# Performance work log

Hardware: AMD Instinct MI355X
Metric: run time of the kernel (lower is better)

The kernel has to match this reference:

```python
import jax, jax.numpy as jnp
import numpy as np

N_NODES = 50000
N_EDGES = 1_600_000
IN_C, HID_C, OUT_C = 512, 256, 50
ALPHA = 0.1
NUM_LAYERS = 10


def setup_inputs() -> dict:
    key = jax.random.key(0)
    ks = jax.random.split(key, 8)
    x = jax.random.normal(ks[0], (N_NODES, IN_C), dtype=jnp.float32)
    edge_row = jax.random.randint(ks[1], (N_EDGES,), 0, N_NODES, dtype=jnp.int32)
    edge_col = jax.random.randint(ks[2], (N_EDGES,), 0, N_NODES, dtype=jnp.int32)
    edge_weight = jax.random.uniform(ks[3], (N_EDGES,), dtype=jnp.float32)
    s1 = 1.0 / np.sqrt(IN_C)
    s2 = 1.0 / np.sqrt(HID_C)
    W1 = jax.random.uniform(ks[4], (IN_C, HID_C), minval=-s1, maxval=s1, dtype=jnp.float32)
    b1 = jax.random.uniform(ks[5], (HID_C,), minval=-s1, maxval=s1, dtype=jnp.float32)
    W2 = jax.random.uniform(ks[6], (HID_C, OUT_C), minval=-s2, maxval=s2, dtype=jnp.float32)
    b2 = jax.random.uniform(ks[7], (OUT_C,), minval=-s2, maxval=s2, dtype=jnp.float32)
    return {"x": x, "edge_row": edge_row, "edge_col": edge_col,
            "edge_weight": edge_weight, "W1": W1, "b1": b1, "W2": W2, "b2": b2}


def reference(x, edge_row, edge_col, edge_weight, W1, b1, W2, b2):
    # MLP: Linear -> ReLU -> Linear (dropout inactive in eval, no batch norm)
    h = jax.nn.relu(x @ W1 + b1)          # [N, HID_C]
    h = h @ W2 + b2                        # [N, OUT_C]
    x0 = h

    def spmm(v):
        # out[i] = sum_{e: row[e]==i} w[e] * v[col[e]]
        msgs = v[edge_col] * edge_weight[:, None]   # [E, OUT_C]
        return jax.ops.segment_sum(msgs, edge_row, num_segments=N_NODES)

    def step(h, _):
        h = spmm(h) * (1.0 - ALPHA) + ALPHA * x0
        return h, None

    h, _ = jax.lax.scan(step, h, None, length=NUM_LAYERS)
    return jax.nn.log_softmax(h, axis=1)
```

## Files before the change

kernel.cpp:

```cpp
#include <hip/hip_runtime.h>
#include <cstddef>
#include <cstdint>
#include <math.h>

#define N_NODES 50000
#define N_EDGES 1600000
#define IN_C 512
#define HID_C 256
#define OUT_C 50
#define PAD_C 64
#define NUM_LAYERS 10
#define NBUCK 98
#define BSHIFT 9
#define BCAP 20480
#define PHB_CHUNK 8192
#define PHB_BLOCKS 196

typedef __attribute__((ext_vector_type(8))) short short8;
typedef __attribute__((ext_vector_type(4))) float floatx4;

__device__ inline unsigned short f2bf(float f) {
    unsigned int u = __float_as_uint(f);
    u += 0x7fffu + ((u >> 16) & 1u);
    return (unsigned short)(u >> 16);
}

__device__ inline unsigned cvtpk(float lo, float hi) {
    unsigned r;
    asm("v_cvt_pk_bf16_f32 %0, %1, %2" : "=v"(r) : "v"(lo), "v"(hi));
    return r;
}

__device__ inline short8 pack_bf16x8(float4 lo, float4 hi) {
    union { unsigned u[4]; short8 s; } r;
    r.u[0] = cvtpk(lo.x, lo.y);
    r.u[1] = cvtpk(lo.z, lo.w);
    r.u[2] = cvtpk(hi.x, hi.y);
    r.u[3] = cvtpk(hi.z, hi.w);
    return r.s;
}

#define ASYNC16(g, l)                                                     \
    __builtin_amdgcn_global_load_lds(                                     \
        (const __attribute__((address_space(1))) void*)(g),               \
        (__attribute__((address_space(3))) void*)(l), 16, 0, 0)

#define WAITCNT6() asm volatile("s_waitcnt vmcnt(6)" ::: "memory")
#define WAITCNT0() asm volatile("s_waitcnt vmcnt(0)" ::: "memory")
#define SBAR()     __builtin_amdgcn_s_barrier()

__global__ __launch_bounds__(256) void transpose_w1(const float* __restrict__ W1,
                                                    unsigned short* __restrict__ Wt) {
    __shared__ float tile[32][33];
    int bx = blockIdx.x;
    int by = blockIdx.y;
    int tx = threadIdx.x & 31, ty = threadIdx.x >> 5;
#pragma unroll
    for (int i = 0; i < 32; i += 8)
        tile[ty + i][tx] = W1[(bx * 32 + ty + i) * HID_C + by * 32 + tx];
    __syncthreads();
#pragma unroll
    for (int i = 0; i < 32; i += 8)
        Wt[(size_t)(by * 32 + ty + i) * IN_C + bx * 32 + tx] = f2bf(tile[tx][ty + i]);
}

__global__ void pad_w2(const float* __restrict__ W2, const float* __restrict__ b2,
                       unsigned short* __restrict__ Wpt, float* __restrict__ bp) {
    int idx = blockIdx.x * blockDim.x + threadIdx.x;
    if (idx < PAD_C * HID_C) {
        int n = idx >> 8, k = idx & 255;
        float v = (n < OUT_C) ? W2[k * OUT_C + n] : 0.f;
        Wpt[idx] = f2bf(v);
    }
    if (idx < PAD_C) bp[idx] = (idx < OUT_C) ? b2[idx] : 0.f;
}

__global__ __launch_bounds__(256) void gemm1_fused(const float* __restrict__ A,
                                                   const unsigned short* __restrict__ Wt,
                                                   const float* __restrict__ b1,
                                                   const unsigned short* __restrict__ Wpt,
                                                   const float* __restrict__ bp,
                                                   float* __restrict__ h0f,
                                                   unsigned short* __restrict__ h0b) {
    __shared__ __align__(16) char smem[73728];
    float*          Ab[3] = {(float*)smem,
                             (float*)(smem + 24576),
                             (float*)(smem + 49152)};
    unsigned short* Bb[3] = {(unsigned short*)(smem + 8192),
                             (unsigned short*)(smem + 32768),
                             (unsigned short*)(smem + 57344)};
    unsigned short* Hs = (unsigned short*)smem;
    const int HS_LD = 264;

    const int tid  = threadIdx.x;
    const int wave = tid >> 6, lane = tid & 63;
    const int quad = lane >> 4, l16 = lane & 15;
    const int m0 = blockIdx.x * 64;
    const int wm = (wave >> 1) * 32;
    const int wn = (wave & 1) * 128;

    floatx4 acc[2][8];
#pragma unroll
    for (int i = 0; i < 2; ++i)
#pragma unroll
        for (int j = 0; j < 8; ++j) acc[i][j] = (floatx4){0.f, 0.f, 0.f, 0.f};

    const int ar = (tid >> 3), ac = tid & 7;
    auto stage = [&](int bi, int ks) {
        const int k0 = ks << 5;
#pragma unroll
        for (int j = 0; j < 2; ++j) {
            int slot = tid + j * 256;
            int r = slot >> 3, c = slot & 7;
            int gr = m0 + r;
            if (gr >= N_NODES) gr = N_NODES - 1;
            const float* src = A + (size_t)gr * IN_C + k0 + ((c ^ (r & 7)) << 2);
            ASYNC16(src, Ab[bi] + (slot << 2));
        }
#pragma unroll
        for (int j = 0; j < 4; ++j) {
            const unsigned short* src = Wt + (size_t)tid * IN_C + k0 + (j << 3);
            ASYNC16(src, Bb[bi] + (j << 11) + (tid << 3));
        }
    };

    auto compute = [&](int bi) {
        const float* As_ = Ab[bi];
        const unsigned short* Bs_ = Bb[bi];
        short8 bfr[8], afr[2];
#pragma unroll
        for (int nt = 0; nt < 8; ++nt)
            bfr[nt] = *(const short8*)&Bs_[(quad << 11) + ((wn + nt * 16 + l16) << 3)];
#pragma unroll
        for (int mt = 0; mt < 2; ++mt) {
            int r  = wm + mt * 16 + l16;
            int rx = r & 7;
            float4 lo = *(const float4*)&As_[(r << 5) + (((2 * quad)     ^ rx) << 2)];
            float4 hi = *(const float4*)&As_[(r << 5) + (((2 * quad + 1) ^ rx) << 2)];
            afr[mt] = pack_bf16x8(lo, hi);
        }
#pragma unroll
        for (int mt = 0; mt < 2; ++mt)
#pragma unroll
            for (int nt = 0; nt < 8; ++nt)
                acc[mt][nt] = __builtin_amdgcn_mfma_f32_16x16x32_bf16(afr[mt], bfr[nt],
                                                                      acc[mt][nt], 0, 0, 0);
    };

    stage(0, 0);
    stage(1, 1);
#pragma unroll
    for (int ks = 0; ks < 14; ++ks) {
        WAITCNT6();
        SBAR();
        stage((ks + 2) % 3, ks + 2);
        compute(ks % 3);
    }
    WAITCNT6(); SBAR(); compute(2);
    WAITCNT0(); SBAR(); compute(0);
    __syncthreads();

#pragma unroll
    for (int nt = 0; nt < 8; ++nt) {
        int n = wn + nt * 16 + l16;
        float bn = b1[n];
#pragma unroll
        for (int mt = 0; mt < 2; ++mt)
#pragma unroll
            for (int r = 0; r < 4; ++r) {
                float v = acc[mt][nt][r] + bn;
                v = v > 0.f ? v : 0.f;
                Hs[(wm + mt * 16 + quad * 4 + r) * HS_LD + n] = f2bf(v);
            }
    }
    __syncthreads();

    floatx4 acc2[4];
#pragma unroll
    for (int nt = 0; nt < 4; ++nt) acc2[nt] = (floatx4){0.f, 0.f, 0.f, 0.f};
    const int hrow = (wave << 4) + l16;
#pragma unroll
    for (int k2 = 0; k2 < 8; ++k2) {
        short8 haf = *(const short8*)&Hs[hrow * HS_LD + (k2 << 5) + (quad << 3)];
#pragma unroll
        for (int nt = 0; nt < 4; ++nt) {
            short8 bf = *(const short8*)&Wpt[(size_t)((nt << 4) + l16) * HID_C + (k2 << 5) + (quad << 3)];
            acc2[nt] = __builtin_amdgcn_mfma_f32_16x16x32_bf16(haf, bf, acc2[nt], 0, 0, 0);
        }
    }
#pragma unroll
    for (int nt = 0; nt < 4; ++nt) {
        int c = (nt << 4) + l16;
        float bn = bp[c];
#pragma unroll
        for (int r = 0; r < 4; ++r) {
            int row = m0 + (wave << 4) + (quad << 2) + r;
            if (row < N_NODES) {
                float v = acc2[nt][r] + bn;
                h0f[(size_t)row * PAD_C + c] = v;
                h0b[(size_t)row * PAD_C + c] = f2bf(v);
            }
        }
    }
}

__global__ __launch_bounds__(256) void bucket_scatter(const int* __restrict__ erow,
                                                      const int* __restrict__ ecol,
                                                      const float* __restrict__ ew,
                                                      int* __restrict__ bfill,
                                                      uint2* __restrict__ buckets) {
    __shared__ int lcnt[NBUCK];
    __shared__ int lbase[NBUCK];
    const int t = threadIdx.x;
    for (int b = t; b < NBUCK; b += 256) lcnt[b] = 0;
    __syncthreads();
    const int e0 = blockIdx.x * PHB_CHUNK;
    const int e1 = min(e0 + PHB_CHUNK, N_EDGES);
    for (int e = e0 + t; e < e1; e += 256)
        atomicAdd(&lcnt[erow[e] >> BSHIFT], 1);
    __syncthreads();
    for (int b = t; b < NBUCK; b += 256) {
        lbase[b] = atomicAdd(&bfill[b], lcnt[b]);
        lcnt[b] = 0;
    }
    __syncthreads();
    for (int e = e0 + t; e < e1; e += 256) {
        int r = erow[e];
        int b = r >> BSHIFT;
        int o = atomicAdd(&lcnt[b], 1);
        int idx = lbase[b] + o;
        if (idx < BCAP) {
            unsigned packed = ((unsigned)(r - (b << BSHIFT)) << 17) | (unsigned)ecol[e];
            buckets[(size_t)b * BCAP + idx] = make_uint2(packed, __float_as_uint(ew[e]));
        }
    }
}

__global__ __launch_bounds__(128) void bucket_scan(const int* __restrict__ bfill,
                                                   int* __restrict__ bbase,
                                                   int* __restrict__ rowptr) {
    __shared__ int sd[128];
    int t = threadIdx.x;
    int v = (t < NBUCK) ? min(bfill[t], BCAP) : 0;
    sd[t] = v;
    __syncthreads();
    for (int off = 1; off < 128; off <<= 1) {
        int x = (t >= off) ? sd[t - off] : 0;
        __syncthreads();
        sd[t] += x;
        __syncthreads();
    }
    if (t < NBUCK) bbase[t] = sd[t] - v;
    if (t == NBUCK - 1) {
        bbase[NBUCK] = sd[t];
        rowptr[N_NODES] = sd[t];
    }
}

__global__ __launch_bounds__(256) void bucket_csr(const uint2* __restrict__ buckets,
                                                  const int* __restrict__ bfill,
                                                  const int* __restrict__ bbase,
                                                  int* __restrict__ rowptr,
                                                  uint2* __restrict__ edges) {
    __shared__ int hist[512];
    __shared__ int excl[512];
    __shared__ int psum[256];
    const int b = blockIdx.x;
    const int t = threadIdx.x;
    const int n = min(bfill[b], BCAP);
    const uint2* bk = buckets + (size_t)b * BCAP;

    hist[t] = 0; hist[t + 256] = 0;
    __syncthreads();
    for (int i = t; i < n; i += 256)
        atomicAdd(&hist[bk[i].x >> 17], 1);
    __syncthreads();
    int a0 = hist[2 * t], a1 = hist[2 * t + 1];
    psum[t] = a0 + a1;
    __syncthreads();
    for (int off = 1; off < 256; off <<= 1) {
        int x = (t >= off) ? psum[t - off] : 0;
        __syncthreads();
        psum[t] += x;
        __syncthreads();
    }
    int pe = psum[t] - (a0 + a1);
    excl[2 * t] = pe;
    excl[2 * t + 1] = pe + a0;
    __syncthreads();
    const int base = bbase[b];
#pragma unroll
    for (int k = 0; k < 2; ++k) {
        int lr = t + k * 256;
        int r = (b << BSHIFT) + lr;
        if (r < N_NODES) rowptr[r] = base + excl[lr];
    }
    hist[t] = 0; hist[t + 256] = 0;
    __syncthreads();
    for (int i = t; i < n; i += 256) {
        uint2 ed = bk[i];
        int lr = ed.x >> 17;
        int pos = base + excl[lr] + atomicAdd(&hist[lr], 1);
        edges[pos] = make_uint2(ed.x & 0x1FFFFu, ed.y);
    }
}

__device__ inline void edge_fma(float* acc, float wgt, uint4 hv) {
    acc[0] = fmaf(wgt, __uint_as_float(hv.x << 16),         acc[0]);
    acc[1] = fmaf(wgt, __uint_as_float(hv.x & 0xffff0000u), acc[1]);
    acc[2] = fmaf(wgt, __uint_as_float(hv.y << 16),         acc[2]);
    acc[3] = fmaf(wgt, __uint_as_float(hv.y & 0xffff0000u), acc[3]);
    acc[4] = fmaf(wgt, __uint_as_float(hv.z << 16),         acc[4]);
    acc[5] = fmaf(wgt, __uint_as_float(hv.z & 0xffff0000u), acc[5]);
    acc[6] = fmaf(wgt, __uint_as_float(hv.w << 16),         acc[6]);
    acc[7] = fmaf(wgt, __uint_as_float(hv.w & 0xffff0000u), acc[7]);
}

template <bool LAST>
__global__ __launch_bounds__(256) void prop8(const int* __restrict__ rowptr,
                                             const uint2* __restrict__ edges,
                                             const unsigned short* __restrict__ hin,
                                             const float* __restrict__ h0f,
                                             unsigned short* __restrict__ hout_b,
                                             float* __restrict__ out_f) {
    int wid = (blockIdx.x * blockDim.x + threadIdx.x) >> 6;
    if (wid >= N_NODES) return;
    int lane = threadIdx.x & 63;
    int slot = lane >> 3;
    int lc   = lane & 7;
    int s = rowptr[wid], e = rowptr[wid + 1];

    float acc0[8], acc1[8];
#pragma unroll
    for (int k = 0; k < 8; ++k) { acc0[k] = 0.f; acc1[k] = 0.f; }

    int i = s;
    for (; i + 32 <= e; i += 32) {
        uint2 cw0 = edges[i + slot];
        uint2 cw1 = edges[i + 8 + slot];
        uint2 cw2 = edges[i + 16 + slot];
        uint2 cw3 = edges[i + 24 + slot];
        uint4 hv0 = *(const uint4*)((const char*)hin + ((size_t)cw0.x << 7) + lc * 16);
        uint4 hv1 = *(const uint4*)((const char*)hin + ((size_t)cw1.x << 7) + lc * 16);
        uint4 hv2 = *(const uint4*)((const char*)hin + ((size_t)cw2.x << 7) + lc * 16);
        uint4 hv3 = *(const uint4*)((const char*)hin + ((size_t)cw3.x << 7) + lc * 16);
        edge_fma(acc0, __uint_as_float(cw0.y), hv0);
        edge_fma(acc1, __uint_as_float(cw1.y), hv1);
        edge_fma(acc0, __uint_as_float(cw2.y), hv2);
        edge_fma(acc1, __uint_as_float(cw3.y), hv3);
    }
    for (; i + 16 <= e; i += 16) {
        uint2 cw0 = edges[i + slot];
        uint2 cw1 = edges[i + 8 + slot];
        uint4 hv0 = *(const uint4*)((const char*)hin + ((size_t)cw0.x << 7) + lc * 16);
        uint4 hv1 = *(const uint4*)((const char*)hin + ((size_t)cw1.x << 7) + lc * 16);
        edge_fma(acc0, __uint_as_float(cw0.y), hv0);
        edge_fma(acc1, __uint_as_float(cw1.y), hv1);
    }
    for (; i < e; i += 8) {
        int idx = i + slot;
        uint2 cw = (idx < e) ? edges[idx] : make_uint2(0u, 0u);
        float wgt = (idx < e) ? __uint_as_float(cw.y) : 0.f;
        uint4 hv = *(const uint4*)((const char*)hin + ((size_t)cw.x << 7) + lc * 16);
        edge_fma(acc0, wgt, hv);
    }

    float r[8];
#pragma unroll
    for (int k = 0; k < 8; ++k) {
        float v = acc0[k] + acc1[k];
        v += __shfl_xor(v, 8, 64);
        v += __shfl_xor(v, 16, 64);
        v += __shfl_xor(v, 32, 64);
        r[k] = v;
    }

    size_t off = (size_t)wid * PAD_C + lc * 8;
    float4 h0a = *(const float4*)(h0f + off);
    float4 h0b4 = *(const float4*)(h0f + off + 4);
    r[0] = 0.9f * r[0] + 0.1f * h0a.x;  r[1] = 0.9f * r[1] + 0.1f * h0a.y;
    r[2] = 0.9f * r[2] + 0.1f * h0a.z;  r[3] = 0.9f * r[3] + 0.1f * h0a.w;
    r[4] = 0.9f * r[4] + 0.1f * h0b4.x; r[5] = 0.9f * r[5] + 0.1f * h0b4.y;
    r[6] = 0.9f * r[6] + 0.1f * h0b4.z; r[7] = 0.9f * r[7] + 0.1f * h0b4.w;

    if (!LAST) {
        if (slot == 0) {
            uint4 u;
            u.x = ((unsigned)f2bf(r[1]) << 16) | f2bf(r[0]);
            u.y = ((unsigned)f2bf(r[3]) << 16) | f2bf(r[2]);
            u.z = ((unsigned)f2bf(r[5]) << 16) | f2bf(r[4]);
            u.w = ((unsigned)f2bf(r[7]) << 16) | f2bf(r[6]);
            *(uint4*)((char*)hout_b + ((size_t)wid << 7) + lc * 16) = u;
        }
    } else {
        int ch0 = lc * 8;
        float m = -INFINITY;
#pragma unroll
        for (int k = 0; k < 8; ++k) if (ch0 + k < OUT_C) m = fmaxf(m, r[k]);
        m = fmaxf(m, __shfl_xor(m, 1, 64));
        m = fmaxf(m, __shfl_xor(m, 2, 64));
        m = fmaxf(m, __shfl_xor(m, 4, 64));
        float ss = 0.f;
#pragma unroll
        for (int k = 0; k < 8; ++k) if (ch0 + k < OUT_C) ss += __expf(r[k] - m);
        ss += __shfl_xor(ss, 1, 64);
        ss += __shfl_xor(ss, 2, 64);
        ss += __shfl_xor(ss, 4, 64);
        float lse = __logf(ss);
        if (slot == 0) {
#pragma unroll
            for (int k = 0; k < 8; ++k)
                if (ch0 + k < OUT_C)
                    out_f[(size_t)wid * OUT_C + ch0 + k] = (r[k] - m) - lse;
        }
    }
}

extern "C" void kernel_launch(void* const* d_in, const int* in_sizes, int n_in,
                              void* d_out, int out_size, void* d_ws, size_t ws_size,
                              hipStream_t stream) {
    const float* x    = (const float*)d_in[0];
    const int*   erow = (const int*)d_in[1];
    const int*   ecol = (const int*)d_in[2];
    const float* ew   = (const float*)d_in[3];
    const float* W1   = (const float*)d_in[4];
    const float* b1   = (const float*)d_in[5];
    const float* W2   = (const float*)d_in[6];
    const float* b2   = (const float*)d_in[7];
    float* out = (float*)d_out;

    char* p = (char*)d_ws;
    auto alloc = [&](size_t bytes) {
        char* r = p;
        p += (bytes + 255) & ~(size_t)255;
        return r;
    };
    char*  scratch = alloc((size_t)NBUCK * BCAP * 8);
    float* h0f    = (float*)alloc((size_t)N_NODES * PAD_C * 4);
    unsigned short* h0b = (unsigned short*)alloc((size_t)N_NODES * PAD_C * 2);
    uint2* edges  = (uint2*)alloc((size_t)N_EDGES * 8);
    int*   rowptr = (int*)alloc((size_t)(N_NODES + 1) * 4);
    int*   bfill  = (int*)alloc((size_t)NBUCK * 4);
    int*   bbase  = (int*)alloc((size_t)(NBUCK + 1) * 4);
    float* bp     = (float*)alloc((size_t)PAD_C * 4);
    unsigned short* Wt  = (unsigned short*)alloc((size_t)HID_C * IN_C * 2);
    unsigned short* Wpt = (unsigned short*)alloc((size_t)PAD_C * HID_C * 2);
    uint2* buckets = (uint2*)scratch;
    unsigned short* ha = (unsigned short*)scratch;
    unsigned short* hb = (unsigned short*)(scratch + (size_t)N_NODES * PAD_C * 2);

    hipMemsetAsync(bfill, 0, (size_t)NBUCK * 4, stream);

    bucket_scatter<<<PHB_BLOCKS, 256, 0, stream>>>(erow, ecol, ew, bfill, buckets);
    bucket_scan<<<1, 128, 0, stream>>>(bfill, bbase, rowptr);
    bucket_csr<<<NBUCK, 256, 0, stream>>>(buckets, bfill, bbase, rowptr, edges);

    transpose_w1<<<dim3(IN_C / 32, HID_C / 32), 256, 0, stream>>>(W1, Wt);
    pad_w2<<<(PAD_C * HID_C + 255) / 256, 256, 0, stream>>>(W2, b2, Wpt, bp);
    gemm1_fused<<<(N_NODES + 63) / 64, 256, 0, stream>>>(x, Wt, b1, Wpt, bp, h0f, h0b);

    const int prop_blocks = (N_NODES * 64 + 255) / 256;
    const unsigned short* cur = h0b;
    unsigned short* nxt = ha;
    for (int l = 0; l < NUM_LAYERS - 1; ++l) {
        prop8<false><<<prop_blocks, 256, 0, stream>>>(rowptr, edges, cur, h0f,
                                                      nxt, nullptr);
        const unsigned short* t = nxt;
        nxt = (nxt == ha) ? hb : ha;
        cur = t;
    }
    prop8<true><<<prop_blocks, 256, 0, stream>>>(rowptr, edges, cur, h0f,
                                                 nullptr, out);
}
```

Before: 624.6 us.

## Split propagation features into two 32-channel halves processed by separate passes

Stores the bf16 feature table as two 32-channel halves and runs each non-final propagation layer as two kernels, one per half. The aim is a 3.2 MB gather table per pass that fits better in cache, with 64-byte rows instead of 128-byte rows. In exchange every layer reads the edge list twice and launches twice as many kernels. The change also swizzles the W1 tile layout in shared memory to cut bank conflicts and switches edge reads to nontemporal loads.

New measurement: 850.3 us. 36.1% more time.

```diff
diff --git a/kernel.cpp b/kernel.cpp
--- a/kernel.cpp
+++ b/kernel.cpp
@@ -9,6 +9,7 @@
 #define HID_C 256
 #define OUT_C 50
 #define PAD_C 64
+#define HALF_C 32
 #define NUM_LAYERS 10
 #define NBUCK 98
 #define BSHIFT 9
@@ -81,7 +82,8 @@
                                                    const unsigned short* __restrict__ Wpt,
                                                    const float* __restrict__ bp,
                                                    float* __restrict__ h0f,
-                                                   unsigned short* __restrict__ h0b) {
+                                                   unsigned short* __restrict__ hA0,
+                                                   unsigned short* __restrict__ hB0) {
     __shared__ __align__(16) char smem[73728];
     float*          Ab[3] = {(float*)smem,
                              (float*)(smem + 24576),
@@ -105,7 +107,6 @@
 #pragma unroll
         for (int j = 0; j < 8; ++j) acc[i][j] = (floatx4){0.f, 0.f, 0.f, 0.f};
 
-    const int ar = (tid >> 3), ac = tid & 7;
     auto stage = [&](int bi, int ks) {
         const int k0 = ks << 5;
 #pragma unroll
@@ -119,8 +120,11 @@
         }
 #pragma unroll
         for (int j = 0; j < 4; ++j) {
-            const unsigned short* src = Wt + (size_t)tid * IN_C + k0 + (j << 3);
-            ASYNC16(src, Bb[bi] + (j << 11) + (tid << 3));
+            int slot = tid + j * 256;
+            int n = slot >> 2, c = slot & 3;
+            int cs = c ^ ((n >> 1) & 3);
+            const unsigned short* src = Wt + (size_t)n * IN_C + k0 + (cs << 3);
+            ASYNC16(src, Bb[bi] + (slot << 3));
         }
     };
 
@@ -129,8 +133,11 @@
         const unsigned short* Bs_ = Bb[bi];
         short8 bfr[8], afr[2];
 #pragma unroll
-        for (int nt = 0; nt < 8; ++nt)
-            bfr[nt] = *(const short8*)&Bs_[(quad << 11) + ((wn + nt * 16 + l16) << 3)];
+        for (int nt = 0; nt < 8; ++nt) {
+            int n  = wn + nt * 16 + l16;
+            int cq = quad ^ ((n >> 1) & 3);
+            bfr[nt] = *(const short8*)&Bs_[(n << 5) + (cq << 3)];
+        }
 #pragma unroll
         for (int mt = 0; mt < 2; ++mt) {
             int r  = wm + mt * 16 + l16;
@@ -198,7 +205,9 @@
             if (row < N_NODES) {
                 float v = acc2[nt][r] + bn;
                 h0f[(size_t)row * PAD_C + c] = v;
-                h0b[(size_t)row * PAD_C + c] = f2bf(v);
+                unsigned short vb = f2bf(v);
+                if (c < HALF_C) hA0[(size_t)row * HALF_C + c] = vb;
+                else            hB0[(size_t)row * HALF_C + (c - HALF_C)] = vb;
             }
         }
     }
@@ -316,52 +325,104 @@
     acc[7] = fmaf(wgt, __uint_as_float(hv.w & 0xffff0000u), acc[7]);
 }
 
-template <bool LAST>
-__global__ __launch_bounds__(256) void prop8(const int* __restrict__ rowptr,
-                                             const uint2* __restrict__ edges,
-                                             const unsigned short* __restrict__ hin,
-                                             const float* __restrict__ h0f,
-                                             unsigned short* __restrict__ hout_b,
-                                             float* __restrict__ out_f) {
+__global__ __launch_bounds__(256) void prop_half(const int* __restrict__ rowptr,
+                                                 const uint2* __restrict__ edges,
+                                                 const unsigned short* __restrict__ hin,
+                                                 const float* __restrict__ h0f,
+                                                 const int hoff,
+                                                 unsigned short* __restrict__ hout) {
+    int wid = (blockIdx.x * blockDim.x + threadIdx.x) >> 6;
+    if (wid >= N_NODES) return;
+    int lane = threadIdx.x & 63;
+    int slot = lane >> 2;
+    int lc2  = lane & 3;
+    int s = rowptr[wid], e = rowptr[wid + 1];
+    const unsigned long long* e8 = (const unsigned long long*)edges;
+
+    float acc0[8], acc1[8];
+#pragma unroll
+    for (int k = 0; k < 8; ++k) { acc0[k] = 0.f; acc1[k] = 0.f; }
+
+    int i = s;
+    for (; i + 32 <= e; i += 32) {
+        unsigned long long c0 = __builtin_nontemporal_load(e8 + i + slot);
+        unsigned long long c1 = __builtin_nontemporal_load(e8 + i + 16 + slot);
+        uint4 hv0 = *(const uint4*)((const char*)hin + (((size_t)(unsigned)c0) << 6) + lc2 * 16);
+        uint4 hv1 = *(const uint4*)((const char*)hin + (((size_t)(unsigned)c1) << 6) + lc2 * 16);
+        edge_fma(acc0, __uint_as_float((unsigned)(c0 >> 32)), hv0);
+        edge_fma(acc1, __uint_as_float((unsigned)(c1 >> 32)), hv1);
+    }
+    for (; i < e; i += 16) {
+        int idx = i + slot;
+        unsigned long long c0 = (idx < e) ? __builtin_nontemporal_load(e8 + idx) : 0ull;
+        float wgt = (idx < e) ? __uint_as_float((unsigned)(c0 >> 32)) : 0.f;
+        uint4 hv = *(const uint4*)((const char*)hin + (((size_t)(unsigned)c0) << 6) + lc2 * 16);
+        edge_fma(acc0, wgt, hv);
+    }
+
+    float r[8];
+#pragma unroll
+    for (int k = 0; k < 8; ++k) {
+        float v = acc0[k] + acc1[k];
+        v += __shfl_xor(v, 4, 64);
+        v += __shfl_xor(v, 8, 64);
+        v += __shfl_xor(v, 16, 64);
+        v += __shfl_xor(v, 32, 64);
+        r[k] = v;
+    }
+
+    size_t off = (size_t)wid * PAD_C + hoff + lc2 * 8;
+    float4 h0a  = *(const float4*)(h0f + off);
+    float4 h0b4 = *(const float4*)(h0f + off + 4);
+    r[0] = 0.9f * r[0] + 0.1f * h0a.x;  r[1] = 0.9f * r[1] + 0.1f * h0a.y;
+    r[2] = 0.9f * r[2] + 0.1f * h0a.z;  r[3] = 0.9f * r[3] + 0.1f * h0a.w;
+    r[4] = 0.9f * r[4] + 0.1f * h0b4.x; r[5] = 0.9f * r[5] + 0.1f * h0b4.y;
+    r[6] = 0.9f * r[6] + 0.1f * h0b4.z; r[7] = 0.9f * r[7] + 0.1f * h0b4.w;
+
+    if (slot == 0) {
+        uint4 u;
+        u.x = ((unsigned)f2bf(r[1]) << 16) | f2bf(r[0]);
+        u.y = ((unsigned)f2bf(r[3]) << 16) | f2bf(r[2]);
+        u.z = ((unsigned)f2bf(r[5]) << 16) | f2bf(r[4]);
+        u.w = ((unsigned)f2bf(r[7]) << 16) | f2bf(r[6]);
+        *(uint4*)((char*)hout + ((size_t)wid << 6) + lc2 * 16) = u;
+    }
+}
+
+__global__ __launch_bounds__(256) void prop_last(const int* __restrict__ rowptr,
+                                                 const uint2* __restrict__ edges,
+                                                 const unsigned short* __restrict__ hinA,
+                                                 const unsigned short* __restrict__ hinB,
+                                                 const float* __restrict__ h0f,
+                                                 float* __restrict__ out_f) {
     int wid = (blockIdx.x * blockDim.x + threadIdx.x) >> 6;
     if (wid >= N_NODES) return;
     int lane = threadIdx.x & 63;
     int slot = lane >> 3;
     int lc   = lane & 7;
+    const unsigned short* hbase = (lc < 4) ? hinA : hinB;
+    const int lco = lc & 3;
     int s = rowptr[wid], e = rowptr[wid + 1];
+    const unsigned long long* e8 = (const unsigned long long*)edges;
 
     float acc0[8], acc1[8];
 #pragma unroll
     for (int k = 0; k < 8; ++k) { acc0[k] = 0.f; acc1[k] = 0.f; }
 
     int i = s;
-    for (; i + 32 <= e; i += 32) {
-        uint2 cw0 = edges[i + slot];
-        uint2 cw1 = edges[i + 8 + slot];
-        uint2 cw2 = edges[i + 16 + slot];
-        uint2 cw3 = edges[i + 24 + slot];
-        uint4 hv0 = *(const uint4*)((const char*)hin + ((size_t)cw0.x << 7) + lc * 16);
-        uint4 hv1 = *(const uint4*)((const char*)hin + ((size_t)cw1.x << 7) + lc * 16);
-        uint4 hv2 = *(const uint4*)((const char*)hin + ((size_t)cw2.x << 7) + lc * 16);
-        uint4 hv3 = *(const uint4*)((const char*)hin + ((size_t)cw3.x << 7) + lc * 16);
-        edge_fma(acc0, __uint_as_float(cw0.y), hv0);
-        edge_fma(acc1, __uint_as_float(cw1.y), hv1);
-        edge_fma(acc0, __uint_as_float(cw2.y), hv2);
-        edge_fma(acc1, __uint_as_float(cw3.y), hv3);
-    }
     for (; i + 16 <= e; i += 16) {
-        uint2 cw0 = edges[i + slot];
-        uint2 cw1 = edges[i + 8 + slot];
-        uint4 hv0 = *(const uint4*)((const char*)hin + ((size_t)cw0.x << 7) + lc * 16);
-        uint4 hv1 = *(const uint4*)((const char*)hin + ((size_t)cw1.x << 7) + lc * 16);
-        edge_fma(acc0, __uint_as_float(cw0.y), hv0);
-        edge_fma(acc1, __uint_as_float(cw1.y), hv1);
+        unsigned long long c0 = __builtin_nontemporal_load(e8 + i + slot);
+        unsigned long long c1 = __builtin_nontemporal_load(e8 + i + 8 + slot);
+        uint4 hv0 = *(const uint4*)((const char*)hbase + (((size_t)(unsigned)c0) << 6) + lco * 16);
+        uint4 hv1 = *(const uint4*)((const char*)hbase + (((size_t)(unsigned)c1) << 6) + lco * 16);
+        edge_fma(acc0, __uint_as_float((unsigned)(c0 >> 32)), hv0);
+        edge_fma(acc1, __uint_as_float((unsigned)(c1 >> 32)), hv1);
     }
     for (; i < e; i += 8) {
         int idx = i + slot;
-        uint2 cw = (idx < e) ? edges[idx] : make_uint2(0u, 0u);
-        float wgt = (idx < e) ? __uint_as_float(cw.y) : 0.f;
-        uint4 hv = *(const uint4*)((const char*)hin + ((size_t)cw.x << 7) + lc * 16);
+        unsigned long long c0 = (idx < e) ? __builtin_nontemporal_load(e8 + idx) : 0ull;
+        float wgt = (idx < e) ? __uint_as_float((unsigned)(c0 >> 32)) : 0.f;
+        uint4 hv = *(const uint4*)((const char*)hbase + (((size_t)(unsigned)c0) << 6) + lco * 16);
         edge_fma(acc0, wgt, hv);
     }
 
@@ -376,43 +437,32 @@
     }
 
     size_t off = (size_t)wid * PAD_C + lc * 8;
-    float4 h0a = *(const float4*)(h0f + off);
+    float4 h0a  = *(const float4*)(h0f + off);
     float4 h0b4 = *(const float4*)(h0f + off + 4);
     r[0] = 0.9f * r[0] + 0.1f * h0a.x;  r[1] = 0.9f * r[1] + 0.1f * h0a.y;
     r[2] = 0.9f * r[2] + 0.1f * h0a.z;  r[3] = 0.9f * r[3] + 0.1f * h0a.w;
     r[4] = 0.9f * r[4] + 0.1f * h0b4.x; r[5] = 0.9f * r[5] + 0.1f * h0b4.y;
     r[6] = 0.9f * r[6] + 0.1f * h0b4.z; r[7] = 0.9f * r[7] + 0.1f * h0b4.w;
 
-    if (!LAST) {
-        if (slot == 0) {
-            uint4 u;
-            u.x = ((unsigned)f2bf(r[1]) << 16) | f2bf(r[0]);
-            u.y = ((unsigned)f2bf(r[3]) << 16) | f2bf(r[2]);
-            u.z = ((unsigned)f2bf(r[5]) << 16) | f2bf(r[4]);
-            u.w = ((unsigned)f2bf(r[7]) << 16) | f2bf(r[6]);
-            *(uint4*)((char*)hout_b + ((size_t)wid << 7) + lc * 16) = u;
-        }
-    } else {
-        int ch0 = lc * 8;
-        float m = -INFINITY;
-#pragma unroll
-        for (int k = 0; k < 8; ++k) if (ch0 + k < OUT_C) m = fmaxf(m, r[k]);
-        m = fmaxf(m, __shfl_xor(m, 1, 64));
-        m = fmaxf(m, __shfl_xor(m, 2, 64));
-        m = fmaxf(m, __shfl_xor(m, 4, 64));
-        float ss = 0.f;
-#pragma unroll
-        for (int k = 0; k < 8; ++k) if (ch0 + k < OUT_C) ss += __expf(r[k] - m);
-        ss += __shfl_xor(ss, 1, 64);
-        ss += __shfl_xor(ss, 2, 64);
-        ss += __shfl_xor(ss, 4, 64);
-        float lse = __logf(ss);
-        if (slot == 0) {
-#pragma unroll
-            for (int k = 0; k < 8; ++k)
-                if (ch0 + k < OUT_C)
-                    out_f[(size_t)wid * OUT_C + ch0 + k] = (r[k] - m) - lse;
-        }
+    int ch0 = lc * 8;
+    float m = -INFINITY;
+#pragma unroll
+    for (int k = 0; k < 8; ++k) if (ch0 + k < OUT_C) m = fmaxf(m, r[k]);
+    m = fmaxf(m, __shfl_xor(m, 1, 64));
+    m = fmaxf(m, __shfl_xor(m, 2, 64));
+    m = fmaxf(m, __shfl_xor(m, 4, 64));
+    float ss = 0.f;
+#pragma unroll
+    for (int k = 0; k < 8; ++k) if (ch0 + k < OUT_C) ss += __expf(r[k] - m);
+    ss += __shfl_xor(ss, 1, 64);
+    ss += __shfl_xor(ss, 2, 64);
+    ss += __shfl_xor(ss, 4, 64);
+    float lse = __logf(ss);
+    if (slot == 0) {
+#pragma unroll
+        for (int k = 0; k < 8; ++k)
+            if (ch0 + k < OUT_C)
+                out_f[(size_t)wid * OUT_C + ch0 + k] = (r[k] - m) - lse;
     }
 }
 
@@ -435,9 +485,9 @@
         p += (bytes + 255) & ~(size_t)255;
         return r;
     };
+    const size_t HTAB = (size_t)N_NODES * HALF_C * 2;
     char*  scratch = alloc((size_t)NBUCK * BCAP * 8);
     float* h0f    = (float*)alloc((size_t)N_NODES * PAD_C * 4);
-    unsigned short* h0b = (unsigned short*)alloc((size_t)N_NODES * PAD_C * 2);
     uint2* edges  = (uint2*)alloc((size_t)N_EDGES * 8);
     int*   rowptr = (int*)alloc((size_t)(N_NODES + 1) * 4);
     int*   bfill  = (int*)alloc((size_t)NBUCK * 4);
@@ -446,8 +496,10 @@
     unsigned short* Wt  = (unsigned short*)alloc((size_t)HID_C * IN_C * 2);
     unsigned short* Wpt = (unsigned short*)alloc((size_t)PAD_C * HID_C * 2);
     uint2* buckets = (uint2*)scratch;
-    unsigned short* ha = (unsigned short*)scratch;
-    unsigned short* hb = (unsigned short*)(scratch + (size_t)N_NODES * PAD_C * 2);
+    unsigned short* hAt[2] = {(unsigned short*)scratch,
+                              (unsigned short*)(scratch + HTAB)};
+    unsigned short* hBt[2] = {(unsigned short*)(scratch + 2 * HTAB),
+                              (unsigned short*)(scratch + 3 * HTAB)};
 
     hipMemsetAsync(bfill, 0, (size_t)NBUCK * 4, stream);
 
@@ -457,18 +509,19 @@
 
     transpose_w1<<<dim3(IN_C / 32, HID_C / 32), 256, 0, stream>>>(W1, Wt);
     pad_w2<<<(PAD_C * HID_C + 255) / 256, 256, 0, stream>>>(W2, b2, Wpt, bp);
-    gemm1_fused<<<(N_NODES + 63) / 64, 256, 0, stream>>>(x, Wt, b1, Wpt, bp, h0f, h0b);
+    gemm1_fused<<<(N_NODES + 63) / 64, 256, 0, stream>>>(x, Wt, b1, Wpt, bp,
+                                                         h0f, hAt[0], hBt[0]);
 
     const int prop_blocks = (N_NODES * 64 + 255) / 256;
-    const unsigned short* cur = h0b;
-    unsigned short* nxt = ha;
+    int cur = 0;
     for (int l = 0; l < NUM_LAYERS - 1; ++l) {
-        prop8<false><<<prop_blocks, 256, 0, stream>>>(rowptr, edges, cur, h0f,
-                                                      nxt, nullptr);
-        const unsigned short* t = nxt;
-        nxt = (nxt == ha) ? hb : ha;
-        cur = t;
-    }
-    prop8<true><<<prop_blocks, 256, 0, stream>>>(rowptr, edges, cur, h0f,
-                                                 nullptr, out);
-}
+        int nxt = cur ^ 1;
+        prop_half<<<prop_blocks, 256, 0, stream>>>(rowptr, edges, hAt[cur], h0f,
+                                                   0, hAt[nxt]);
+        prop_half<<<prop_blocks, 256, 0, stream>>>(rowptr, edges, hBt[cur], h0f,
+                                                   HALF_C, hBt[nxt]);
+        cur = nxt;
+    }
+    prop_last<<<prop_blocks, 256, 0, stream>>>(rowptr, edges, hAt[cur], hBt[cur],
+                                               h0f, out);
+}
```

## Fuse ten propagation layers into one persistent kernel with grid barriers

Applied to the files above, without the earlier changes.

Replaces the ten per-layer prop8 launches with a single persistent kernel of 1024 blocks that loops over the layers. Waves stride over nodes, and blocks synchronise between layers through an atomic-counter grid barrier. The teacher term now reads the bf16 h0 instead of the fp32 h0, and the W1 shared-memory tile layout gets an XOR swizzle. This removes launch overhead and per-layer tail gaps, but adds barrier spin cost and depends on all blocks being co-resident; using bf16 h0 also costs a little precision.

Measured after the change: 2.285 ms. 3.66x slower.

```diff
diff --git a/kernel.cpp b/kernel.cpp
--- a/kernel.cpp
+++ b/kernel.cpp
@@ -15,6 +15,8 @@
 #define BCAP 20480
 #define PHB_CHUNK 8192
 #define PHB_BLOCKS 196
+#define PROP_BLOCKS 1024
+#define PROP_WAVES (PROP_BLOCKS * 4)
 
 typedef __attribute__((ext_vector_type(8))) short short8;
 typedef __attribute__((ext_vector_type(4))) float floatx4;
@@ -105,7 +107,6 @@
 #pragma unroll
         for (int j = 0; j < 8; ++j) acc[i][j] = (floatx4){0.f, 0.f, 0.f, 0.f};
 
-    const int ar = (tid >> 3), ac = tid & 7;
     auto stage = [&](int bi, int ks) {
         const int k0 = ks << 5;
 #pragma unroll
@@ -119,8 +120,11 @@
         }
 #pragma unroll
         for (int j = 0; j < 4; ++j) {
-            const unsigned short* src = Wt + (size_t)tid * IN_C + k0 + (j << 3);
-            ASYNC16(src, Bb[bi] + (j << 11) + (tid << 3));
+            int slot = tid + j * 256;
+            int n = slot >> 2, c = slot & 3;
+            int cs = c ^ ((n >> 1) & 3);
+            const unsigned short* src = Wt + (size_t)n * IN_C + k0 + (cs << 3);
+            ASYNC16(src, Bb[bi] + (slot << 3));
         }
     };
 
@@ -129,8 +133,11 @@
         const unsigned short* Bs_ = Bb[bi];
         short8 bfr[8], afr[2];
 #pragma unroll
-        for (int nt = 0; nt < 8; ++nt)
-            bfr[nt] = *(const short8*)&Bs_[(quad << 11) + ((wn + nt * 16 + l16) << 3)];
+        for (int nt = 0; nt < 8; ++nt) {
+            int n  = wn + nt * 16 + l16;
+            int cq = quad ^ ((n >> 1) & 3);
+            bfr[nt] = *(const short8*)&Bs_[(n << 5) + (cq << 3)];
+        }
 #pragma unroll
         for (int mt = 0; mt < 2; ++mt) {
             int r  = wm + mt * 16 + l16;
@@ -316,102 +323,129 @@
     acc[7] = fmaf(wgt, __uint_as_float(hv.w & 0xffff0000u), acc[7]);
 }
 
-template <bool LAST>
-__global__ __launch_bounds__(256) void prop8(const int* __restrict__ rowptr,
-                                             const uint2* __restrict__ edges,
-                                             const unsigned short* __restrict__ hin,
-                                             const float* __restrict__ h0f,
-                                             unsigned short* __restrict__ hout_b,
-                                             float* __restrict__ out_f) {
-    int wid = (blockIdx.x * blockDim.x + threadIdx.x) >> 6;
-    if (wid >= N_NODES) return;
-    int lane = threadIdx.x & 63;
-    int slot = lane >> 3;
-    int lc   = lane & 7;
-    int s = rowptr[wid], e = rowptr[wid + 1];
-
-    float acc0[8], acc1[8];
-#pragma unroll
-    for (int k = 0; k < 8; ++k) { acc0[k] = 0.f; acc1[k] = 0.f; }
-
-    int i = s;
-    for (; i + 32 <= e; i += 32) {
-        uint2 cw0 = edges[i + slot];
-        uint2 cw1 = edges[i + 8 + slot];
-        uint2 cw2 = edges[i + 16 + slot];
-        uint2 cw3 = edges[i + 24 + slot];
-        uint4 hv0 = *(const uint4*)((const char*)hin + ((size_t)cw0.x << 7) + lc * 16);
-        uint4 hv1 = *(const uint4*)((const char*)hin + ((size_t)cw1.x << 7) + lc * 16);
-        uint4 hv2 = *(const uint4*)((const char*)hin + ((size_t)cw2.x << 7) + lc * 16);
-        uint4 hv3 = *(const uint4*)((const char*)hin + ((size_t)cw3.x << 7) + lc * 16);
-        edge_fma(acc0, __uint_as_float(cw0.y), hv0);
-        edge_fma(acc1, __uint_as_float(cw1.y), hv1);
-        edge_fma(acc0, __uint_as_float(cw2.y), hv2);
-        edge_fma(acc1, __uint_as_float(cw3.y), hv3);
-    }
-    for (; i + 16 <= e; i += 16) {
-        uint2 cw0 = edges[i + slot];
-        uint2 cw1 = edges[i + 8 + slot];
-        uint4 hv0 = *(const uint4*)((const char*)hin + ((size_t)cw0.x << 7) + lc * 16);
-        uint4 hv1 = *(const uint4*)((const char*)hin + ((size_t)cw1.x << 7) + lc * 16);
-        edge_fma(acc0, __uint_as_float(cw0.y), hv0);
-        edge_fma(acc1, __uint_as_float(cw1.y), hv1);
-    }
-    for (; i < e; i += 8) {
-        int idx = i + slot;
-        uint2 cw = (idx < e) ? edges[idx] : make_uint2(0u, 0u);
-        float wgt = (idx < e) ? __uint_as_float(cw.y) : 0.f;
-        uint4 hv = *(const uint4*)((const char*)hin + ((size_t)cw.x << 7) + lc * 16);
-        edge_fma(acc0, wgt, hv);
-    }
-
-    float r[8];
-#pragma unroll
-    for (int k = 0; k < 8; ++k) {
-        float v = acc0[k] + acc1[k];
-        v += __shfl_xor(v, 8, 64);
-        v += __shfl_xor(v, 16, 64);
-        v += __shfl_xor(v, 32, 64);
-        r[k] = v;
-    }
-
-    size_t off = (size_t)wid * PAD_C + lc * 8;
-    float4 h0a = *(const float4*)(h0f + off);
-    float4 h0b4 = *(const float4*)(h0f + off + 4);
-    r[0] = 0.9f * r[0] + 0.1f * h0a.x;  r[1] = 0.9f * r[1] + 0.1f * h0a.y;
-    r[2] = 0.9f * r[2] + 0.1f * h0a.z;  r[3] = 0.9f * r[3] + 0.1f * h0a.w;
-    r[4] = 0.9f * r[4] + 0.1f * h0b4.x; r[5] = 0.9f * r[5] + 0.1f * h0b4.y;
-    r[6] = 0.9f * r[6] + 0.1f * h0b4.z; r[7] = 0.9f * r[7] + 0.1f * h0b4.w;
-
-    if (!LAST) {
-        if (slot == 0) {
-            uint4 u;
-            u.x = ((unsigned)f2bf(r[1]) << 16) | f2bf(r[0]);
-            u.y = ((unsigned)f2bf(r[3]) << 16) | f2bf(r[2]);
-            u.z = ((unsigned)f2bf(r[5]) << 16) | f2bf(r[4]);
-            u.w = ((unsigned)f2bf(r[7]) << 16) | f2bf(r[6]);
-            *(uint4*)((char*)hout_b + ((size_t)wid << 7) + lc * 16) = u;
-        }
-    } else {
-        int ch0 = lc * 8;
-        float m = -INFINITY;
-#pragma unroll
-        for (int k = 0; k < 8; ++k) if (ch0 + k < OUT_C) m = fmaxf(m, r[k]);
-        m = fmaxf(m, __shfl_xor(m, 1, 64));
-        m = fmaxf(m, __shfl_xor(m, 2, 64));
-        m = fmaxf(m, __shfl_xor(m, 4, 64));
-        float ss = 0.f;
-#pragma unroll
-        for (int k = 0; k < 8; ++k) if (ch0 + k < OUT_C) ss += __expf(r[k] - m);
-        ss += __shfl_xor(ss, 1, 64);
-        ss += __shfl_xor(ss, 2, 64);
-        ss += __shfl_xor(ss, 4, 64);
-        float lse = __logf(ss);
-        if (slot == 0) {
-#pragma unroll
-            for (int k = 0; k < 8; ++k)
-                if (ch0 + k < OUT_C)
-                    out_f[(size_t)wid * OUT_C + ch0 + k] = (r[k] - m) - lse;
+__global__ __launch_bounds__(256, 4) void prop_fused(const int* __restrict__ rowptr,
+                                                     const uint2* __restrict__ edges,
+                                                     const unsigned short* __restrict__ h0b,
+                                                     unsigned short* __restrict__ ha,
+                                                     unsigned short* __restrict__ hb,
+                                                     int* __restrict__ bar,
+                                                     float* __restrict__ out_f) {
+    const int wslot = (blockIdx.x * blockDim.x + threadIdx.x) >> 6;
+    const int lane = threadIdx.x & 63;
+    const int slot = lane >> 3;
+    const int lc   = lane & 7;
+
+    const unsigned short* cur = h0b;
+    unsigned short* nxt = ha;
+
+    for (int l = 0; l < NUM_LAYERS; ++l) {
+        const bool last = (l == NUM_LAYERS - 1);
+        for (int wid = wslot; wid < N_NODES; wid += PROP_WAVES) {
+            int s = rowptr[wid], e = rowptr[wid + 1];
+
+            float acc0[8], acc1[8];
+#pragma unroll
+            for (int k = 0; k < 8; ++k) { acc0[k] = 0.f; acc1[k] = 0.f; }
+
+            int i = s;
+            for (; i + 32 <= e; i += 32) {
+                uint2 cw0 = edges[i + slot];
+                uint2 cw1 = edges[i + 8 + slot];
+                uint2 cw2 = edges[i + 16 + slot];
+                uint2 cw3 = edges[i + 24 + slot];
+                uint4 hv0 = *(const uint4*)((const char*)cur + ((size_t)cw0.x << 7) + lc * 16);
+                uint4 hv1 = *(const uint4*)((const char*)cur + ((size_t)cw1.x << 7) + lc * 16);
+                uint4 hv2 = *(const uint4*)((const char*)cur + ((size_t)cw2.x << 7) + lc * 16);
+                uint4 hv3 = *(const uint4*)((const char*)cur + ((size_t)cw3.x << 7) + lc * 16);
+                edge_fma(acc0, __uint_as_float(cw0.y), hv0);
+                edge_fma(acc1, __uint_as_float(cw1.y), hv1);
+                edge_fma(acc0, __uint_as_float(cw2.y), hv2);
+                edge_fma(acc1, __uint_as_float(cw3.y), hv3);
+            }
+            for (; i + 16 <= e; i += 16) {
+                uint2 cw0 = edges[i + slot];
+                uint2 cw1 = edges[i + 8 + slot];
+                uint4 hv0 = *(const uint4*)((const char*)cur + ((size_t)cw0.x << 7) + lc * 16);
+                uint4 hv1 = *(const uint4*)((const char*)cur + ((size_t)cw1.x << 7) + lc * 16);
+                edge_fma(acc0, __uint_as_float(cw0.y), hv0);
+                edge_fma(acc1, __uint_as_float(cw1.y), hv1);
+            }
+            for (; i < e; i += 8) {
+                int idx = i + slot;
+                uint2 cw = (idx < e) ? edges[idx] : make_uint2(0u, 0u);
+                float wgt = (idx < e) ? __uint_as_float(cw.y) : 0.f;
+                uint4 hv = *(const uint4*)((const char*)cur + ((size_t)cw.x << 7) + lc * 16);
+                edge_fma(acc0, wgt, hv);
+            }
+
+            float r[8];
+#pragma unroll
+            for (int k = 0; k < 8; ++k) {
+                float v = acc0[k] + acc1[k];
+                v += __shfl_xor(v, 8, 64);
+                v += __shfl_xor(v, 16, 64);
+                v += __shfl_xor(v, 32, 64);
+                r[k] = v;
+            }
+
+            uint4 h0v = *(const uint4*)((const char*)h0b + ((size_t)wid << 7) + lc * 16);
+            float h0e[8];
+            h0e[0] = __uint_as_float(h0v.x << 16);
+            h0e[1] = __uint_as_float(h0v.x & 0xffff0000u);
+            h0e[2] = __uint_as_float(h0v.y << 16);
+            h0e[3] = __uint_as_float(h0v.y & 0xffff0000u);
+            h0e[4] = __uint_as_float(h0v.z << 16);
+            h0e[5] = __uint_as_float(h0v.z & 0xffff0000u);
+            h0e[6] = __uint_as_float(h0v.w << 16);
+            h0e[7] = __uint_as_float(h0v.w & 0xffff0000u);
+#pragma unroll
+            for (int k = 0; k < 8; ++k) r[k] = 0.9f * r[k] + 0.1f * h0e[k];
+
+            if (!last) {
+                if (slot == 0) {
+                    uint4 u;
+                    u.x = ((unsigned)f2bf(r[1]) << 16) | f2bf(r[0]);
+                    u.y = ((unsigned)f2bf(r[3]) << 16) | f2bf(r[2]);
+                    u.z = ((unsigned)f2bf(r[5]) << 16) | f2bf(r[4]);
+                    u.w = ((unsigned)f2bf(r[7]) << 16) | f2bf(r[6]);
+                    *(uint4*)((char*)nxt + ((size_t)wid << 7) + lc * 16) = u;
+                }
+            } else {
+                int ch0 = lc * 8;
+                float m = -INFINITY;
+#pragma unroll
+                for (int k = 0; k < 8; ++k) if (ch0 + k < OUT_C) m = fmaxf(m, r[k]);
+                m = fmaxf(m, __shfl_xor(m, 1, 64));
+                m = fmaxf(m, __shfl_xor(m, 2, 64));
+                m = fmaxf(m, __shfl_xor(m, 4, 64));
+                float ss = 0.f;
+#pragma unroll
+                for (int k = 0; k < 8; ++k) if (ch0 + k < OUT_C) ss += __expf(r[k] - m);
+                ss += __shfl_xor(ss, 1, 64);
+                ss += __shfl_xor(ss, 2, 64);
+                ss += __shfl_xor(ss, 4, 64);
+                float lse = __logf(ss);
+                if (slot == 0) {
+#pragma unroll
+                    for (int k = 0; k < 8; ++k)
+                        if (ch0 + k < OUT_C)
+                            out_f[(size_t)wid * OUT_C + ch0 + k] = (r[k] - m) - lse;
+                }
+            }
+        }
+        if (!last) {
+            __syncthreads();
+            if (threadIdx.x == 0) {
+                __threadfence();
+                atomicAdd(&bar[l], 1);
+                while (__hip_atomic_load(&bar[l], __ATOMIC_ACQUIRE,
+                                         __HIP_MEMORY_SCOPE_AGENT) < PROP_BLOCKS)
+                    __builtin_amdgcn_s_sleep(8);
+                __threadfence();
+            }
+            __syncthreads();
+            cur = nxt;
+            nxt = (nxt == ha) ? hb : ha;
         }
     }
 }
@@ -442,6 +476,7 @@
     int*   rowptr = (int*)alloc((size_t)(N_NODES + 1) * 4);
     int*   bfill  = (int*)alloc((size_t)NBUCK * 4);
     int*   bbase  = (int*)alloc((size_t)(NBUCK + 1) * 4);
+    int*   bar    = (int*)alloc((size_t)16 * 4);
     float* bp     = (float*)alloc((size_t)PAD_C * 4);
     unsigned short* Wt  = (unsigned short*)alloc((size_t)HID_C * IN_C * 2);
     unsigned short* Wpt = (unsigned short*)alloc((size_t)PAD_C * HID_C * 2);
@@ -450,6 +485,7 @@
     unsigned short* hb = (unsigned short*)(scratch + (size_t)N_NODES * PAD_C * 2);
 
     hipMemsetAsync(bfill, 0, (size_t)NBUCK * 4, stream);
+    hipMemsetAsync(bar, 0, (size_t)16 * 4, stream);
 
     bucket_scatter<<<PHB_BLOCKS, 256, 0, stream>>>(erow, ecol, ew, bfill, buckets);
     bucket_scan<<<1, 128, 0, stream>>>(bfill, bbase, rowptr);
@@ -459,16 +495,5 @@
     pad_w2<<<(PAD_C * HID_C + 255) / 256, 256, 0, stream>>>(W2, b2, Wpt, bp);
     gemm1_fused<<<(N_NODES + 63) / 64, 256, 0, stream>>>(x, Wt, b1, Wpt, bp, h0f, h0b);
 
-    const int prop_blocks = (N_NODES * 64 + 255) / 256;
-    const unsigned short* cur = h0b;
-    unsigned short* nxt = ha;
-    for (int l = 0; l < NUM_LAYERS - 1; ++l) {
-        prop8<false><<<prop_blocks, 256, 0, stream>>>(rowptr, edges, cur, h0f,
-                                                      nxt, nullptr);
-        const unsigned short* t = nxt;
-        nxt = (nxt == ha) ? hb : ha;
-        cur = t;
-    }
-    prop8<true><<<prop_blocks, 256, 0, stream>>>(rowptr, edges, cur, h0f,
-                                                 nullptr, out);
-}
+    prop_fused<<<PROP_BLOCKS, 256, 0, stream>>>(rowptr, edges, h0b, ha, hb, bar, out);
+}
```

## Drop fp32 x0 copy, swizzle B tile in LDS, add prop occupancy hint

Applied to the files above, without the earlier changes.

The fp32 copy of the MLP output is removed. The teleport term in each propagation layer now reads the bf16 copy, which halves those bytes and removes one large write from the GEMM. The W1 tile staging in LDS gets an XOR swizzle so that B-fragment loads spread across banks. prop8 also gets a launch-bounds occupancy hint of 8 blocks, at some risk of register pressure, and x0 now enters each layer at bf16 precision, which costs some accuracy.

New measurement: 594.6 us. 1.05x faster.

```diff
diff --git a/kernel.cpp b/kernel.cpp
--- a/kernel.cpp
+++ b/kernel.cpp
@@ -80,7 +80,6 @@
                                                    const float* __restrict__ b1,
                                                    const unsigned short* __restrict__ Wpt,
                                                    const float* __restrict__ bp,
-                                                   float* __restrict__ h0f,
                                                    unsigned short* __restrict__ h0b) {
     __shared__ __align__(16) char smem[73728];
     float*          Ab[3] = {(float*)smem,
@@ -105,7 +104,6 @@
 #pragma unroll
         for (int j = 0; j < 8; ++j) acc[i][j] = (floatx4){0.f, 0.f, 0.f, 0.f};
 
-    const int ar = (tid >> 3), ac = tid & 7;
     auto stage = [&](int bi, int ks) {
         const int k0 = ks << 5;
 #pragma unroll
@@ -119,8 +117,11 @@
         }
 #pragma unroll
         for (int j = 0; j < 4; ++j) {
-            const unsigned short* src = Wt + (size_t)tid * IN_C + k0 + (j << 3);
-            ASYNC16(src, Bb[bi] + (j << 11) + (tid << 3));
+            int slot = tid + j * 256;
+            int n = slot >> 2, c = slot & 3;
+            int cs = c ^ ((n >> 1) & 3);
+            const unsigned short* src = Wt + (size_t)n * IN_C + k0 + (cs << 3);
+            ASYNC16(src, Bb[bi] + (slot << 3));
         }
     };
 
@@ -129,8 +130,11 @@
         const unsigned short* Bs_ = Bb[bi];
         short8 bfr[8], afr[2];
 #pragma unroll
-        for (int nt = 0; nt < 8; ++nt)
-            bfr[nt] = *(const short8*)&Bs_[(quad << 11) + ((wn + nt * 16 + l16) << 3)];
+        for (int nt = 0; nt < 8; ++nt) {
+            int n  = wn + nt * 16 + l16;
+            int cq = quad ^ ((n >> 1) & 3);
+            bfr[nt] = *(const short8*)&Bs_[(n << 5) + (cq << 3)];
+        }
 #pragma unroll
         for (int mt = 0; mt < 2; ++mt) {
             int r  = wm + mt * 16 + l16;
@@ -195,11 +199,8 @@
 #pragma unroll
         for (int r = 0; r < 4; ++r) {
             int row = m0 + (wave << 4) + (quad << 2) + r;
-            if (row < N_NODES) {
-                float v = acc2[nt][r] + bn;
-                h0f[(size_t)row * PAD_C + c] = v;
-                h0b[(size_t)row * PAD_C + c] = f2bf(v);
-            }
+            if (row < N_NODES)
+                h0b[(size_t)row * PAD_C + c] = f2bf(acc2[nt][r] + bn);
         }
     }
 }
@@ -317,12 +318,12 @@
 }
 
 template <bool LAST>
-__global__ __launch_bounds__(256) void prop8(const int* __restrict__ rowptr,
-                                             const uint2* __restrict__ edges,
-                                             const unsigned short* __restrict__ hin,
-                                             const float* __restrict__ h0f,
-                                             unsigned short* __restrict__ hout_b,
-                                             float* __restrict__ out_f) {
+__global__ __launch_bounds__(256, 8) void prop8(const int* __restrict__ rowptr,
+                                                const uint2* __restrict__ edges,
+                                                const unsigned short* __restrict__ hin,
+                                                const unsigned short* __restrict__ h0b,
+                                                unsigned short* __restrict__ hout_b,
+                                                float* __restrict__ out_f) {
     int wid = (blockIdx.x * blockDim.x + threadIdx.x) >> 6;
     if (wid >= N_NODES) return;
     int lane = threadIdx.x & 63;
@@ -375,13 +376,18 @@
         r[k] = v;
     }
 
-    size_t off = (size_t)wid * PAD_C + lc * 8;
-    float4 h0a = *(const float4*)(h0f + off);
-    float4 h0b4 = *(const float4*)(h0f + off + 4);
-    r[0] = 0.9f * r[0] + 0.1f * h0a.x;  r[1] = 0.9f * r[1] + 0.1f * h0a.y;
-    r[2] = 0.9f * r[2] + 0.1f * h0a.z;  r[3] = 0.9f * r[3] + 0.1f * h0a.w;
-    r[4] = 0.9f * r[4] + 0.1f * h0b4.x; r[5] = 0.9f * r[5] + 0.1f * h0b4.y;
-    r[6] = 0.9f * r[6] + 0.1f * h0b4.z; r[7] = 0.9f * r[7] + 0.1f * h0b4.w;
+    uint4 h0v = *(const uint4*)((const char*)h0b + ((size_t)wid << 7) + lc * 16);
+    float h0e[8];
+    h0e[0] = __uint_as_float(h0v.x << 16);
+    h0e[1] = __uint_as_float(h0v.x & 0xffff0000u);
+    h0e[2] = __uint_as_float(h0v.y << 16);
+    h0e[3] = __uint_as_float(h0v.y & 0xffff0000u);
+    h0e[4] = __uint_as_float(h0v.z << 16);
+    h0e[5] = __uint_as_float(h0v.z & 0xffff0000u);
+    h0e[6] = __uint_as_float(h0v.w << 16);
+    h0e[7] = __uint_as_float(h0v.w & 0xffff0000u);
+#pragma unroll
+    for (int k = 0; k < 8; ++k) r[k] = 0.9f * r[k] + 0.1f * h0e[k];
 
     if (!LAST) {
         if (slot == 0) {
@@ -436,7 +442,6 @@
         return r;
     };
     char*  scratch = alloc((size_t)NBUCK * BCAP * 8);
-    float* h0f    = (float*)alloc((size_t)N_NODES * PAD_C * 4);
     unsigned short* h0b = (unsigned short*)alloc((size_t)N_NODES * PAD_C * 2);
     uint2* edges  = (uint2*)alloc((size_t)N_EDGES * 8);
     int*   rowptr = (int*)alloc((size_t)(N_NODES + 1) * 4);
@@ -457,18 +462,18 @@
 
     transpose_w1<<<dim3(IN_C / 32, HID_C / 32), 256, 0, stream>>>(W1, Wt);
     pad_w2<<<(PAD_C * HID_C + 255) / 256, 256, 0, stream>>>(W2, b2, Wpt, bp);
-    gemm1_fused<<<(N_NODES + 63) / 64, 256, 0, stream>>>(x, Wt, b1, Wpt, bp, h0f, h0b);
+    gemm1_fused<<<(N_NODES + 63) / 64, 256, 0, stream>>>(x, Wt, b1, Wpt, bp, h0b);
 
     const int prop_blocks = (N_NODES * 64 + 255) / 256;
     const unsigned short* cur = h0b;
     unsigned short* nxt = ha;
     for (int l = 0; l < NUM_LAYERS - 1; ++l) {
-        prop8<false><<<prop_blocks, 256, 0, stream>>>(rowptr, edges, cur, h0f,
+        prop8<false><<<prop_blocks, 256, 0, stream>>>(rowptr, edges, cur, h0b,
                                                       nxt, nullptr);
         const unsigned short* t = nxt;
         nxt = (nxt == ha) ? hb : ha;
         cur = t;
     }
-    prop8<true><<<prop_blocks, 256, 0, stream>>>(rowptr, edges, cur, h0f,
+    prop8<true><<<prop_blocks, 256, 0, stream>>>(rowptr, edges, cur, h0b,
                                                  nullptr, out);
 }
```
